# Kernel optimization log

Measured on AMD Instinct MI355X. Metric: run time of the kernel, lower is better.

Reference implementation:

```python
import jax, jax.numpy as jnp
import numpy as np

CHUNK = 32
HEADS = 4
EPS_RMS = 1e-5

def silu(x):
    return jax.nn.silu(x)

def l2norm(x, eps=1e-6):
    return x * jax.lax.rsqrt(jnp.sum(x * x, axis=-1, keepdims=True) + eps)

def short_conv(x, w):
    # x: (b, l, c); w: (c, K) depthwise causal conv, no bias
    K = w.shape[1]
    L = x.shape[1]
    xp = jnp.pad(x, ((0, 0), (K - 1, 0), (0, 0)))
    out = xp[:, 0:L, :] * w[:, 0]
    for k in range(1, K):
        out = out + xp[:, k:k + L, :] * w[:, k]
    return out

def delta_rule_chunkwise(q, k, v, beta, chunk=CHUNK):
    # q,k: (b,h,l,dk); v: (b,h,l,dv); beta: (b,h,l). l divisible by chunk.
    b, h, l, dk = q.shape
    dv = v.shape[-1]
    n = l // chunk
    q = l2norm(q)
    k = l2norm(k)
    v = v * beta[..., None]
    k_beta = k * beta[..., None]
    resh = lambda x: x.reshape(b, h, n, chunk, -1)
    q, k, v, k_beta = map(resh, (q, k, v, k_beta))
    strict_lower = jnp.tril(jnp.ones((chunk, chunk), bool), -1)
    # A = -(k_beta k^T) kept strictly lower triangular
    attn = jnp.where(strict_lower, -(k_beta @ jnp.swapaxes(k, -1, -2)), 0.0)
    # forward substitution: T = (I - A)^{-1} - I built row by row (fixed 32 rows)
    for i in range(1, chunk):
        row = attn[..., i, :]                                  # (b,h,n,c)
        new = attn[..., i, :i] + jnp.einsum('...j,...jk->...k', row, attn[..., :, :i])
        attn = attn.at[..., i, :i].set(new)
    attn = attn + jnp.eye(chunk, dtype=attn.dtype)
    u = attn @ v        # (b,h,n,c,dv)
    w = attn @ k_beta   # (b,h,n,c,dk)
    lower_incl = jnp.tril(jnp.ones((chunk, chunk), bool))
    qc, kc, uc, wc = [jnp.moveaxis(x, 2, 0) for x in (q, k, u, w)]
    S0 = jnp.zeros((b, h, dk, dv), q.dtype)
    def step(S, inp):
        q_i, k_i, u_i, w_i = inp
        attn_i = jnp.where(lower_incl, q_i @ jnp.swapaxes(k_i, -1, -2), 0.0)
        u_adj = u_i - w_i @ S
        o_i = q_i @ S + attn_i @ u_adj
        S = S + jnp.swapaxes(k_i, -1, -2) @ u_adj
        return S, o_i
    S, o = jax.lax.scan(step, S0, (qc, kc, uc, wc))
    o = jnp.moveaxis(o, 0, 2).reshape(b, h, l, dv)
    return o, S

def ema_rule(v, gamma):
    # v: (b,h,l,dv), gamma: (b,h,l); sequential EMA scan
    v_t = jnp.moveaxis(v, 2, 0)       # (l,b,h,dv)
    g_t = jnp.moveaxis(gamma, 2, 0)   # (l,b,h)
    s0 = jnp.zeros(v.shape[:2] + (v.shape[-1],), v.dtype)
    def step(s, inp):
        vt, gt = inp
        s = gt[..., None] * s + (1.0 - gt[..., None]) * vt
        return s, s
    s_fin, out = jax.lax.scan(step, s0, (v_t, g_t))
    return jnp.moveaxis(out, 0, 2), s_fin

def rms_norm(x, w, eps=EPS_RMS):
    return x * jax.lax.rsqrt(jnp.mean(x * x, axis=-1, keepdims=True) + eps) * w

def setup_inputs() -> dict:
    key = jax.random.key(0)
    ks = jax.random.split(key, 16)
    b, l, d = 4, 2048, 1024
    H, conv_K = HEADS, 4
    s = 0.02
    return {
        'hidden_states': jax.random.normal(ks[0], (b, l, d), jnp.float32),
        'Wq': jax.random.normal(ks[1], (d, d), jnp.float32) * s,
        'Wk': jax.random.normal(ks[2], (d, d), jnp.float32) * s,
        'Wv': jax.random.normal(ks[3], (d, d), jnp.float32) * s,
        'conv_q': jax.random.normal(ks[4], (d, conv_K), jnp.float32) * 0.3,
        'conv_k': jax.random.normal(ks[5], (d, conv_K), jnp.float32) * 0.3,
        'conv_v': jax.random.normal(ks[6], (d, conv_K), jnp.float32) * 0.3,
        'Wb': jax.random.normal(ks[7], (d, H), jnp.float32) * s,
        'Wdec': jax.random.normal(ks[8], (d, H), jnp.float32) * s,
        'Wmix': jax.random.normal(ks[9], (d, H), jnp.float32) * s,
        'conv_mix': jax.random.normal(ks[10], (H, conv_K), jnp.float32) * 0.3,
        'mix_bias': jnp.full((H,), -2.0, jnp.float32),
        'rms_w': jnp.ones((d // H,), jnp.float32),
        'Wo': jax.random.normal(ks[11], (d, d), jnp.float32) * s,
    }

def reference(hidden_states, Wq, Wk, Wv, conv_q, conv_k, conv_v, Wb, Wdec, Wmix, conv_mix, mix_bias, rms_w, Wo):
    b, l, d = hidden_states.shape
    H = HEADS
    dk = d // H
    dv = d // H
    # projections + causal depthwise short conv (silu activation inside conv)
    q = silu(short_conv(hidden_states @ Wq, conv_q))
    k = silu(short_conv(hidden_states @ Wk, conv_k))
    v = silu(short_conv(hidden_states @ Wv, conv_v))
    mix_inp = silu(short_conv(hidden_states @ Wmix, conv_mix))  # (b,l,H)
    # qk_activation == 'silu' applies an extra silu after conv (per source)
    q = silu(q)
    k = silu(k)
    # split heads -> (b,H,l,dh)
    to_heads = lambda x, dh: jnp.transpose(x.reshape(b, l, H, dh), (0, 2, 1, 3))
    q_d = to_heads(q, dk)
    k_d = to_heads(k, dk)
    v_d = to_heads(v, dv)
    beta = jax.nn.sigmoid(hidden_states @ Wb)           # (b,l,H)
    beta_d = jnp.transpose(beta, (0, 2, 1))             # (b,H,l)
    o_d, S = delta_rule_chunkwise(q_d, k_d, v_d, beta_d)
    o_d = jnp.transpose(o_d, (0, 2, 1, 3))              # (b,l,H,dv)
    # EMA branch
    gamma = jax.nn.sigmoid(hidden_states @ Wdec)        # (b,l,H)
    gamma_d = jnp.transpose(gamma, (0, 2, 1))
    ema_out, ema_state = ema_rule(v_d, gamma_d)
    ema_out = jnp.transpose(ema_out, (0, 2, 1, 3))      # (b,l,H,dv)
    # fine-grained head mix gate
    mix = jax.nn.sigmoid(mix_inp + mix_bias)            # (b,l,H)
    o = (1.0 - mix[..., None]) * o_d + mix[..., None] * ema_out
    # per-head RMSNorm then output projection
    o = rms_norm(o, rms_w)
    out = o.reshape(b, l, H * dv) @ Wo
    return out
```

## Files before the change

### kernel.cpp

```cpp
#include <hip/hip_runtime.h>
#include <hip/hip_bf16.h>

#define B 4
#define L 2048
#define D 1024
#define NH 4
#define DK 256
#define CHUNK 32
#define NCH 64
#define BH (B*NH)
#define ET 64
#define ENCH (L/ET)
#define TB 8

typedef __attribute__((ext_vector_type(8))) __bf16 bf16x8;
typedef __attribute__((ext_vector_type(4))) __bf16 bf16x4;
typedef __attribute__((ext_vector_type(4))) float f32x4;

__device__ inline unsigned short f2bf(float f) {
    union { float f; unsigned u; } v; v.f = f;
    unsigned r = v.u + 0x7fffu + ((v.u >> 16) & 1u);
    return (unsigned short)(r >> 16);
}
__device__ inline float bf2f(unsigned short h) {
    union { unsigned u; float f; } v; v.u = ((unsigned)h) << 16; return v.f;
}
__device__ inline float sigmoidf_(float x) { return 1.0f / (1.0f + __expf(-x)); }
__device__ inline float siluf_(float x) { return x / (1.0f + __expf(-x)); }
__device__ inline unsigned cvt_pk_bf16(float lo, float hi) {
    unsigned r;
    asm("v_cvt_pk_bf16_f32 %0, %1, %2" : "=v"(r) : "v"(lo), "v"(hi));
    return r;
}

#define MFMA16(a, b, c) __builtin_amdgcn_mfma_f32_16x16x32_bf16((a), (b), (c), 0, 0, 0)

__device__ inline void bar_lds() {
    __builtin_amdgcn_s_waitcnt(0xC07F);
    __builtin_amdgcn_s_barrier();
}

__device__ inline void load_lds16(const unsigned short* g, unsigned short* l) {
    __builtin_amdgcn_global_load_lds(
        (const __attribute__((address_space(1))) unsigned int*)g,
        (__attribute__((address_space(3))) unsigned int*)l, 16, 0, 0);
}

__global__ __launch_bounds__(256) void k_wT(const float* Wq, const float* Wk, const float* Wv,
                                            const float* Wo, unsigned short* wT)
{
    __shared__ float tile[32][33];
    int z = blockIdx.z;
    const float* W = (z == 0) ? Wq : (z == 1) ? Wk : (z == 2) ? Wv : Wo;
    unsigned short* out = wT + (size_t)z * D * D;
    int kt = blockIdx.x * 32, nt = blockIdx.y * 32;
    int tx = threadIdx.x & 31, ty = threadIdx.x >> 5;
#pragma unroll
    for (int i = 0; i < 4; i++)
        tile[ty + 8 * i][tx] = W[(size_t)(kt + ty + 8 * i) * D + nt + tx];
    __syncthreads();
#pragma unroll
    for (int i = 0; i < 4; i++)
        out[(size_t)(nt + ty + 8 * i) * D + kt + tx] = f2bf(tile[tx][ty + 8 * i]);
}

__global__ __launch_bounds__(256) void k_cvt(const float* h, unsigned short* hb, int n4)
{
    int i = blockIdx.x * blockDim.x + threadIdx.x;
    int stride = gridDim.x * blockDim.x;
    const float4* h4 = (const float4*)h;
    for (; i < n4; i += stride) {
        float4 v = h4[i];
        ushort4 o;
        o.x = f2bf(v.x); o.y = f2bf(v.y); o.z = f2bf(v.z); o.w = f2bf(v.w);
        *(ushort4*)(hb + 4 * (size_t)i) = o;
    }
}

template<int NTOT, bool OUT_F32>
__global__ __launch_bounds__(256) void k_gemm_lds(const unsigned short* __restrict__ A,
                                                  const unsigned short* __restrict__ BT,
                                                  void* __restrict__ outp)
{
    __shared__ __align__(16) unsigned short As[128 * 32];
    __shared__ __align__(16) unsigned short Bs[128 * 32];
    const int K = 1024;
    int tid = threadIdx.x;
    int w = tid >> 6, lane = tid & 63;
    int r16 = lane & 15, quad = lane >> 4;
    int wm = w & 1, wn = w >> 1;
    int bm = blockIdx.x * 128;
    int bn = blockIdx.y * 128;
    int lrow = lane >> 2;
    int lcol = (lane & 3) * 8;
    f32x4 z4 = {0.f, 0.f, 0.f, 0.f};
    f32x4 acc[4][4];
#pragma unroll
    for (int i = 0; i < 4; i++)
#pragma unroll
        for (int j = 0; j < 4; j++) acc[i][j] = z4;

    for (int kt = 0; kt < K; kt += 32) {
#pragma unroll
        for (int j = 0; j < 2; j++) {
            int r0 = (w * 2 + j) * 16;
            load_lds16(A + (size_t)(bm + r0 + lrow) * K + kt + lcol, &As[r0 * 32]);
            load_lds16(BT + (size_t)(bn + r0 + lrow) * K + kt + lcol, &Bs[r0 * 32]);
        }
        __syncthreads();
        bf16x8 af[4], bf[4];
#pragma unroll
        for (int ms = 0; ms < 4; ms++)
            af[ms] = *(const bf16x8*)&As[(wm * 64 + ms * 16 + r16) * 32 + quad * 8];
#pragma unroll
        for (int ns = 0; ns < 4; ns++)
            bf[ns] = *(const bf16x8*)&Bs[(wn * 64 + ns * 16 + r16) * 32 + quad * 8];
#pragma unroll
        for (int ms = 0; ms < 4; ms++)
#pragma unroll
            for (int ns = 0; ns < 4; ns++)
                acc[ms][ns] = MFMA16(af[ms], bf[ns], acc[ms][ns]);
        __syncthreads();
    }
#pragma unroll
    for (int ms = 0; ms < 4; ms++)
#pragma unroll
        for (int ns = 0; ns < 4; ns++)
#pragma unroll
            for (int r = 0; r < 4; r++) {
                int m = bm + wm * 64 + ms * 16 + quad * 4 + r;
                int n = bn + wn * 64 + ns * 16 + r16;
                if (OUT_F32)
                    ((float*)outp)[(size_t)m * NTOT + n] = acc[ms][ns][r];
                else
                    ((unsigned short*)outp)[(size_t)m * NTOT + n] = f2bf(acc[ms][ns][r]);
            }
}

__global__ __launch_bounds__(256) void k_smallproj(const float* hid, const float* Wb, const float* Wd,
                                                   const float* Wm, float* beta, float* gamma, float* xmix)
{
    int wave = threadIdx.x >> 6, lane = threadIdx.x & 63;
    int row = blockIdx.x * 4 + wave;
    const float* hrow = hid + (size_t)row * D;
    float acc[12];
#pragma unroll
    for (int j = 0; j < 12; j++) acc[j] = 0.f;
    for (int i = 0; i < 16; i++) {
        int k = lane + 64 * i;
        float h = hrow[k];
        float4 wb = ((const float4*)Wb)[k];
        float4 wd = ((const float4*)Wd)[k];
        float4 wm = ((const float4*)Wm)[k];
        acc[0] += h * wb.x; acc[1] += h * wb.y; acc[2] += h * wb.z; acc[3] += h * wb.w;
        acc[4] += h * wd.x; acc[5] += h * wd.y; acc[6] += h * wd.z; acc[7] += h * wd.w;
        acc[8] += h * wm.x; acc[9] += h * wm.y; acc[10] += h * wm.z; acc[11] += h * wm.w;
    }
#pragma unroll
    for (int j = 0; j < 12; j++)
        for (int off = 32; off; off >>= 1) acc[j] += __shfl_xor(acc[j], off, 64);
    if (lane < 4) {
        beta[(size_t)row * 4 + lane] = sigmoidf_(acc[lane]);
        gamma[(size_t)row * 4 + lane] = sigmoidf_(acc[4 + lane]);
        xmix[(size_t)row * 4 + lane] = acc[8 + lane];
    }
}

__global__ __launch_bounds__(256) void k_convnorm(const unsigned short* __restrict__ xqkv,
                                                  const float* __restrict__ cq,
                                                  const float* __restrict__ ck,
                                                  const float* __restrict__ cv,
                                                  unsigned short* __restrict__ qn,
                                                  unsigned short* __restrict__ kn,
                                                  unsigned short* __restrict__ vb)
{
    int blk = blockIdx.x;
    int b = blk >> 8;
    int t0 = (blk & 255) * TB;
    int tid = threadIdx.x;
    int h = tid >> 6, lane = tid & 63;
    int c = tid * 4;

    float wq[4][4], wk[4][4], wv[4][4];
#pragma unroll
    for (int j = 0; j < 4; j++) {
        float4 a = *(const float4*)(cq + (size_t)(c + j) * 4);
        wq[j][0] = a.x; wq[j][1] = a.y; wq[j][2] = a.z; wq[j][3] = a.w;
        float4 d4 = *(const float4*)(ck + (size_t)(c + j) * 4);
        wk[j][0] = d4.x; wk[j][1] = d4.y; wk[j][2] = d4.z; wk[j][3] = d4.w;
        float4 e = *(const float4*)(cv + (size_t)(c + j) * 4);
        wv[j][0] = e.x; wv[j][1] = e.y; wv[j][2] = e.z; wv[j][3] = e.w;
    }

    float aq[4][4], ak[4][4], av[4][4];
#pragma unroll
    for (int s = 0; s < 4; s++)
#pragma unroll
        for (int j = 0; j < 4; j++) { aq[s][j] = 0.f; ak[s][j] = 0.f; av[s][j] = 0.f; }

    const unsigned short* xb = xqkv + (size_t)(b * L) * (3 * D) + c;

#pragma unroll
    for (int p = 0; p < 3; p++) {
        int r = t0 - 3 + p;
        if (r >= 0) {
            const unsigned short* pp = xb + (size_t)r * (3 * D);
            ushort4 xq = *(const ushort4*)pp;
            ushort4 xk = *(const ushort4*)(pp + D);
            ushort4 xv = *(const ushort4*)(pp + 2 * D);
            float fq[4] = {bf2f(xq.x), bf2f(xq.y), bf2f(xq.z), bf2f(xq.w)};
            float fk[4] = {bf2f(xk.x), bf2f(xk.y), bf2f(xk.z), bf2f(xk.w)};
            float fv[4] = {bf2f(xv.x), bf2f(xv.y), bf2f(xv.z), bf2f(xv.w)};
#pragma unroll
            for (int d = 3 - p; d <= 3; d++) {
                int s = (p + d + 1) & 3;
                int kk = 3 - d;
#pragma unroll
                for (int j = 0; j < 4; j++) {
                    aq[s][j] += wq[j][kk] * fq[j];
                    ak[s][j] += wk[j][kk] * fk[j];
                    av[s][j] += wv[j][kk] * fv[j];
                }
            }
        }
    }

    ushort4 sq2[2], sk2[2], sv2[2];
    {
        const unsigned short* pp = xb + (size_t)t0 * (3 * D);
        sq2[0] = *(const ushort4*)pp;
        sk2[0] = *(const ushort4*)(pp + D);
        sv2[0] = *(const ushort4*)(pp + 2 * D);
    }

#pragma unroll
    for (int i = 0; i < TB; i++) {
        if (i + 1 < TB) {
            const unsigned short* pp = xb + (size_t)(t0 + i + 1) * (3 * D);
            sq2[(i + 1) & 1] = *(const ushort4*)pp;
            sk2[(i + 1) & 1] = *(const ushort4*)(pp + D);
            sv2[(i + 1) & 1] = *(const ushort4*)(pp + 2 * D);
        }
        {
            ushort4 xq = sq2[i & 1], xk = sk2[i & 1], xv = sv2[i & 1];
            float fq[4] = {bf2f(xq.x), bf2f(xq.y), bf2f(xq.z), bf2f(xq.w)};
            float fk[4] = {bf2f(xk.x), bf2f(xk.y), bf2f(xk.z), bf2f(xk.w)};
            float fv[4] = {bf2f(xv.x), bf2f(xv.y), bf2f(xv.z), bf2f(xv.w)};
#pragma unroll
            for (int d = 0; d < 4; d++) {
                if (i + d < TB) {
                    int s = (i + d) & 3;
                    int kk = 3 - d;
#pragma unroll
                    for (int j = 0; j < 4; j++) {
                        aq[s][j] += wq[j][kk] * fq[j];
                        ak[s][j] += wk[j][kk] * fk[j];
                        av[s][j] += wv[j][kk] * fv[j];
                    }
                }
            }
        }
        {
            const int s = i & 3;
            float rq[4], rk[4], rv[4];
#pragma unroll
            for (int j = 0; j < 4; j++) {
                rq[j] = siluf_(siluf_(aq[s][j]));
                rk[j] = siluf_(siluf_(ak[s][j]));
                rv[j] = siluf_(av[s][j]);
            }
            float sqs = rq[0] * rq[0] + rq[1] * rq[1] + rq[2] * rq[2] + rq[3] * rq[3];
            float sks = rk[0] * rk[0] + rk[1] * rk[1] + rk[2] * rk[2] + rk[3] * rk[3];
            for (int off = 32; off; off >>= 1) {
                sqs += __shfl_xor(sqs, off, 64);
                sks += __shfl_xor(sks, off, 64);
            }
            float qs = rsqrtf(sqs + 1e-6f), ks = rsqrtf(sks + 1e-6f);
            int t = t0 + i;
            size_t oidx = ((size_t)(b * NH + h) * L + t) * DK + lane * 4;
            ushort4 oq, ok, ov;
            oq.x = f2bf(rq[0] * qs); oq.y = f2bf(rq[1] * qs); oq.z = f2bf(rq[2] * qs); oq.w = f2bf(rq[3] * qs);
            ok.x = f2bf(rk[0] * ks); ok.y = f2bf(rk[1] * ks); ok.z = f2bf(rk[2] * ks); ok.w = f2bf(rk[3] * ks);
            ov.x = f2bf(rv[0]); ov.y = f2bf(rv[1]); ov.z = f2bf(rv[2]); ov.w = f2bf(rv[3]);
            *(ushort4*)(qn + oidx) = oq;
            *(ushort4*)(kn + oidx) = ok;
            *(ushort4*)(vb + (size_t)(b * L + t) * D + c) = ov;
            if (i + 4 < TB) {
#pragma unroll
                for (int j = 0; j < 4; j++) { aq[s][j] = 0.f; ak[s][j] = 0.f; av[s][j] = 0.f; }
            }
        }
    }
}

__global__ __launch_bounds__(256) void k_convmix(const float* xmix, const float* cmix, float* mixinp)
{
    int idx = blockIdx.x * 256 + threadIdx.x;
    int h = idx & 3;
    int t = (idx >> 2) & (L - 1);
    int b = idx >> 13;
    float acc = 0.f;
#pragma unroll
    for (int kk = 0; kk < 4; kk++) {
        int tt = t - 3 + kk;
        if (tt >= 0) acc += cmix[h * 4 + kk] * xmix[((size_t)(b * L + tt) << 2) + h];
    }
    mixinp[idx] = siluf_(acc);
}

#define KTS 40
__global__ __launch_bounds__(256) void k_delta_pre(const unsigned short* qn, const unsigned short* kn,
                                                   const unsigned short* vb, const float* beta,
                                                   unsigned short* wneg, unsigned short* knT,
                                                   unsigned short* attnb, float* u)
{
    __shared__ __align__(16) unsigned short kTl[256 * KTS];
    __shared__ __align__(16) unsigned short vTl[256 * KTS];
    __shared__ __align__(16) unsigned short T2b[32 * KTS];
    __shared__ float Gs[32 * 33];
    int bx = blockIdx.x;
    int bh = bx >> 6, ch = bx & 63;
    int b = bh >> 2, h = bh & 3;
    int t0 = ch * 32;
    int tid = threadIdx.x;
    int w = tid >> 6, lane = tid & 63;
    int r16 = lane & 15, quad = lane >> 4;
    size_t rowbase = (size_t)(bh * L + t0);
    f32x4 z4 = {0.f, 0.f, 0.f, 0.f};

    if (w < 3) {
        int mi = (w == 0) ? 0 : 1;
        int ni = (w == 2) ? 1 : 0;
        const unsigned short* krm = kn + (rowbase + mi * 16 + r16) * DK;
        const unsigned short* krn = kn + (rowbase + ni * 16 + r16) * DK;
        const unsigned short* qrm = qn + (rowbase + mi * 16 + r16) * DK;
        f32x4 g = z4, qk = z4;
#pragma unroll
        for (int kt = 0; kt < 8; kt++) {
            bf16x8 a  = *(const bf16x8*)(krm + kt * 32 + quad * 8);
            bf16x8 bb = *(const bf16x8*)(krn + kt * 32 + quad * 8);
            bf16x8 qa = *(const bf16x8*)(qrm + kt * 32 + quad * 8);
            g  = MFMA16(a, bb, g);
            qk = MFMA16(qa, bb, qk);
        }
#pragma unroll
        for (int r = 0; r < 4; r++) {
            int i = mi * 16 + quad * 4 + r, j = ni * 16 + r16;
            Gs[i * 33 + j] = g[r];
            attnb[(size_t)(bh * 64 + ch) * 1024 + i * 32 + j] =
                (j <= i) ? f2bf(qk[r]) : (unsigned short)0;
        }
    } else {
#pragma unroll
        for (int r = 0; r < 4; r++) {
            int i = quad * 4 + r, j = 16 + r16;
            attnb[(size_t)(bh * 64 + ch) * 1024 + i * 32 + j] = 0;
        }
    }
    {
        int t = tid & 31, c0 = (tid >> 5) * 32;
        const unsigned short* krow = kn + (rowbase + t) * DK + c0;
        const unsigned short* vrow = vb + ((size_t)(b * L + t0 + t)) * D + h * DK + c0;
#pragma unroll
        for (int j = 0; j < 32; j += 4) {
            ushort4 kv = *(const ushort4*)(krow + j);
            ushort4 vv = *(const ushort4*)(vrow + j);
            kTl[(c0 + j + 0) * KTS + t] = kv.x;
            kTl[(c0 + j + 1) * KTS + t] = kv.y;
            kTl[(c0 + j + 2) * KTS + t] = kv.z;
            kTl[(c0 + j + 3) * KTS + t] = kv.w;
            vTl[(c0 + j + 0) * KTS + t] = vv.x;
            vTl[(c0 + j + 1) * KTS + t] = vv.y;
            vTl[(c0 + j + 2) * KTS + t] = vv.z;
            vTl[(c0 + j + 3) * KTS + t] = vv.w;
        }
    }
    __syncthreads();

    if (w == 0) {
        int c = lane & 31;
        float rr[32];
#pragma unroll
        for (int j = 0; j < 32; j++) rr[j] = Gs[j * 33 + c];
        rr[0] = 0.f;
        float bc = beta[(size_t)(b * L + t0 + c) * NH + h];
#pragma unroll
        for (int i = 1; i < 32; i++) {
            float bi = __shfl(bc, i, 64);
            float s = -bi * rr[i];
#pragma unroll
            for (int j = 1; j < i; j++) {
                float aij = -bi * __shfl(rr[i], j, 64);
                s += aij * ((c < j) ? rr[j] : 0.f);
            }
            rr[i] = (c < i) ? s : 0.f;
        }
        if (lane < 32) {
#pragma unroll
            for (int i = 0; i < 32; i++) {
                float val = (rr[i] + ((i == c) ? 1.f : 0.f)) * bc;
                T2b[i * KTS + c] = f2bf(val);
            }
        }
    } else {
        int idx = tid - 64;
        for (int rowc = idx; rowc < 256; rowc += 192) {
            unsigned short* kT = knT + ((size_t)(bh * 64 + ch) * DK + rowc) * 32;
#pragma unroll
            for (int seg = 0; seg < 4; seg++) {
                uint4 d = *(const uint4*)&kTl[rowc * KTS + seg * 8];
                *(uint4*)(kT + seg * 8) = d;
            }
        }
    }
    __syncthreads();

#pragma unroll
    for (int mt = 0; mt < 2; mt++) {
        bf16x8 ta = *(const bf16x8*)&T2b[(mt * 16 + r16) * KTS + quad * 8];
#pragma unroll
        for (int nt2 = 0; nt2 < 4; nt2++) {
            int nt = w * 4 + nt2;
            bf16x8 vb2 = *(const bf16x8*)&vTl[(nt * 16 + r16) * KTS + quad * 8];
            bf16x8 kb = *(const bf16x8*)&kTl[(nt * 16 + r16) * KTS + quad * 8];
            f32x4 uu = MFMA16(ta, vb2, z4);
            f32x4 ww = MFMA16(ta, kb, z4);
            float* ug = u + (rowbase + mt * 16 + quad * 4) * DK + nt * 16 + r16;
            unsigned short* wg = wneg + (rowbase + mt * 16 + quad * 4) * DK + nt * 16 + r16;
#pragma unroll
            for (int r = 0; r < 4; r++) {
                ug[(size_t)r * DK] = uu[r];
                wg[(size_t)r * DK] = f2bf(-ww[r]);
            }
        }
    }
}

__global__ __launch_bounds__(256) void k_ema_local(const unsigned short* v, const float* gamma,
                                                   float* ema_local, float* Acum,
                                                   float* s_end, float* Pchunk)
{
    __shared__ float gsh[ET];
    int blk = blockIdx.x;
    int bh = blk >> 5;
    int ch = blk & (ENCH - 1);
    int b = bh >> 2, h = bh & 3;
    int c = threadIdx.x;
    int t0 = ch * ET;
    if (c < ET) gsh[c] = gamma[(size_t)(b * L + t0 + c) * NH + h];
    __syncthreads();
    const unsigned short* vg = v + (size_t)(b * L + t0) * D + h * DK + c;
    float* eg = ema_local + (size_t)(b * L + t0) * D + h * DK + c;
    float* Ag = Acum + (size_t)bh * L + t0;
    float s = 0.f;
    float A = 1.f;
#pragma unroll 8
    for (int i = 0; i < ET; i++) {
        float g = gsh[i];
        s = g * s + (1.f - g) * bf2f(vg[(size_t)i * D]);
        A *= g;
        eg[(size_t)i * D] = s;
        if (c == 0) Ag[i] = A;
    }
    s_end[((size_t)bh * ENCH + ch) * DK + c] = s;
    if (c == 0) Pchunk[(size_t)bh * ENCH + ch] = A;
}

__global__ __launch_bounds__(256) void k_ema_carry(const float* s_end, const float* Pchunk, float* S_in)
{
    int bh = blockIdx.x;
    int c = threadIdx.x;
    float S = 0.f;
    for (int ch = 0; ch < ENCH; ch++) {
        S_in[((size_t)bh * ENCH + ch) * DK + c] = S;
        float P = Pchunk[(size_t)bh * ENCH + ch];
        S = P * S + s_end[((size_t)bh * ENCH + ch) * DK + c];
    }
}

#define STS 280
#define USTR 40
__global__ __launch_bounds__(128, 1) void k_scan(const unsigned short* __restrict__ qn,
                                                 const unsigned short* __restrict__ wneg,
                                                 const unsigned short* __restrict__ knT,
                                                 const unsigned short* __restrict__ attnb,
                                                 const float* __restrict__ u, float* __restrict__ od)
{
    __shared__ __align__(16) unsigned short st[16 * STS];
    __shared__ __align__(16) unsigned short uat[16 * USTR];
    __shared__ __align__(16) unsigned short sq[2][32 * 256];
    __shared__ __align__(16) unsigned short sw[2][32 * 256];
    int bh = blockIdx.x;
    int tile = blockIdx.y;
    int b = bh >> 2, h = bh & 3;
    int mo = threadIdx.x >> 6, lane = threadIdx.x & 63;
    int n = lane & 15, q = lane >> 4;
    int cbase = tile * 16;
    f32x4 z4 = {0.f, 0.f, 0.f, 0.f};
    f32x4 sacc[8];
#pragma unroll
    for (int a = 0; a < 8; a++) sacc[a] = z4;

    const unsigned short* qb = qn + (size_t)bh * L * DK;
    const unsigned short* wb = wneg + (size_t)bh * L * DK;
    const float* ub = u + (size_t)bh * L * DK;
    const unsigned short* kTbase = knT + (size_t)bh * 64 * DK * 32;
    const unsigned short* atbase = attnb + (size_t)bh * 64 * 1024;
    int dkb = mo * 128;

    int hl = lane >> 5, cc = lane & 31;
    auto stage = [&](int ch, int p) {
        const unsigned short* src = (mo == 0) ? (qb + (size_t)ch * 32 * DK)
                                              : (wb + (size_t)ch * 32 * DK);
        unsigned short* dst = (mo == 0) ? sq[p] : sw[p];
#pragma unroll
        for (int seg = 0; seg < 16; seg++) {
            int row = seg * 2 + hl;
            int scol = cc ^ (row & 7);
            load_lds16(src + (size_t)row * DK + scol * 8, dst + seg * 512);
        }
    };

    f32x4 uB[2];
    auto loadu = [&](int ch, int p) {
        const float* up = ub + (size_t)(ch * 32 + 16 * mo + q * 4) * DK + cbase + n;
        f32x4 a; a[0] = up[0]; a[1] = up[DK]; a[2] = up[2 * DK]; a[3] = up[3 * DK];
        uB[p] = a;
    };

    bf16x8 kf2[2][8], af2[2];
    auto loadkf = [&](int ch, int p) {
        const unsigned short* kTb = kTbase + (size_t)ch * DK * 32;
#pragma unroll
        for (int a = 0; a < 8; a++)
            kf2[p][a] = *(const bf16x8*)(kTb + (size_t)(dkb + a * 16 + n) * 32 + q * 8);
        af2[p] = *(const bf16x8*)(atbase + (size_t)ch * 1024 + (16 * mo + n) * 32 + q * 8);
    };

    stage(0, 0); loadu(0, 0); loadkf(0, 0);

    auto body = [&](int ch, int par) {
        int t0 = ch * 32;
        asm volatile("s_waitcnt vmcnt(0)" ::: "memory");
        if (ch + 1 < NCH) {
            stage(ch + 1, par ^ 1);
            loadu(ch + 1, par ^ 1);
            loadkf(ch + 1, par ^ 1);
        }
#pragma unroll
        for (int a = 0; a < 8; a++) {
            uint2 pk2;
            pk2.x = cvt_pk_bf16(sacc[a][0], sacc[a][1]);
            pk2.y = cvt_pk_bf16(sacc[a][2], sacc[a][3]);
            *(uint2*)&st[n * STS + dkb + a * 16 + q * 4] = pk2;
        }
        bar_lds();

        f32x4 auE = uB[par], auO = z4, aoE = z4, aoO = z4;
        int rowoff = (16 * mo + n) * 256;
        int rsw = n & 7;
#pragma unroll
        for (int kt = 0; kt < 8; kt += 2) {
            bf16x8 s0 = *(const bf16x8*)&st[n * STS + (kt + 0) * 32 + q * 8];
            bf16x8 s1 = *(const bf16x8*)&st[n * STS + (kt + 1) * 32 + q * 8];
            bf16x8 w0 = *(const bf16x8*)&sw[par][rowoff + (((kt + 0) * 4 + q) ^ rsw) * 8];
            bf16x8 q0 = *(const bf16x8*)&sq[par][rowoff + (((kt + 0) * 4 + q) ^ rsw) * 8];
            bf16x8 w1 = *(const bf16x8*)&sw[par][rowoff + (((kt + 1) * 4 + q) ^ rsw) * 8];
            bf16x8 q1 = *(const bf16x8*)&sq[par][rowoff + (((kt + 1) * 4 + q) ^ rsw) * 8];
            auE = MFMA16(w0, s0, auE);
            aoE = MFMA16(q0, s0, aoE);
            auO = MFMA16(w1, s1, auO);
            aoO = MFMA16(q1, s1, aoO);
        }
        f32x4 au = auE + auO;

        {
            uint2 pu;
            pu.x = cvt_pk_bf16(au[0], au[1]);
            pu.y = cvt_pk_bf16(au[2], au[3]);
            *(uint2*)&uat[n * USTR + 16 * mo + q * 4] = pu;
        }
        bar_lds();

        {
            bf16x8 uf = *(const bf16x8*)&uat[n * USTR + q * 8];
            f32x4 ao = aoE + aoO;
            ao = MFMA16(af2[par], uf, ao);
            float* op = od + (size_t)(b * L + t0 + 16 * mo + q * 4) * D + h * DK + cbase + n;
            op[0] = ao[0]; op[D] = ao[1]; op[2 * D] = ao[2]; op[3 * D] = ao[3];
#pragma unroll
            for (int a = 0; a < 8; a++)
                sacc[a] = MFMA16(kf2[par][a], uf, sacc[a]);
        }
    };

    for (int ch2 = 0; ch2 < NCH; ch2 += 2) {
        body(ch2, 0);
        body(ch2 + 1, 1);
    }
}

__global__ __launch_bounds__(256) void k_mixrms(const float* od, const float* ema_local,
                                                const float* Acum, const float* S_in,
                                                const float* mixinp,
                                                const float* mix_bias, const float* rms_w,
                                                unsigned short* onorm)
{
    int row = blockIdx.x;
    int tid = threadIdx.x;
    int h = tid >> 6, lane = tid & 63;
    int b = row >> 11, t = row & (L - 1);
    int bh = b * NH + h;
    int ch = t >> 6;
    float m = sigmoidf_(mixinp[(size_t)row * NH + h] + mix_bias[h]);
    int c = tid * 4;
    float A = Acum[(size_t)bh * L + t];
    float4 sin4 = *(const float4*)(S_in + ((size_t)bh * ENCH + ch) * DK + (c & (DK - 1)));
    float4 o = *(const float4*)(od + (size_t)row * D + c);
    float4 e = *(const float4*)(ema_local + (size_t)row * D + c);
    e.x += A * sin4.x; e.y += A * sin4.y; e.z += A * sin4.z; e.w += A * sin4.w;
    float x0 = o.x + m * (e.x - o.x);
    float x1 = o.y + m * (e.y - o.y);
    float x2 = o.z + m * (e.z - o.z);
    float x3 = o.w + m * (e.w - o.w);
    float ss = x0 * x0 + x1 * x1 + x2 * x2 + x3 * x3;
    for (int off = 32; off; off >>= 1) ss += __shfl_xor(ss, off, 64);
    float scale = rsqrtf(ss * (1.0f / 256.0f) + 1e-5f);
    float4 w = *(const float4*)(rms_w + lane * 4);
    uint2 p;
    p.x = f2bf(x0 * scale * w.x) | ((unsigned)f2bf(x1 * scale * w.y) << 16);
    p.y = f2bf(x2 * scale * w.z) | ((unsigned)f2bf(x3 * scale * w.w) << 16);
    *(uint2*)(onorm + (size_t)row * D + c) = p;
}

extern "C" void kernel_launch(void* const* d_in, const int* in_sizes, int n_in,
                              void* d_out, int out_size, void* d_ws, size_t ws_size,
                              hipStream_t stream)
{
    (void)in_sizes; (void)n_in; (void)out_size; (void)ws_size;
    const float* hidden   = (const float*)d_in[0];
    const float* Wq       = (const float*)d_in[1];
    const float* Wk       = (const float*)d_in[2];
    const float* Wv       = (const float*)d_in[3];
    const float* conv_q   = (const float*)d_in[4];
    const float* conv_k   = (const float*)d_in[5];
    const float* conv_v   = (const float*)d_in[6];
    const float* Wb       = (const float*)d_in[7];
    const float* Wdec     = (const float*)d_in[8];
    const float* Wmix     = (const float*)d_in[9];
    const float* conv_mix = (const float*)d_in[10];
    const float* mix_bias = (const float*)d_in[11];
    const float* rms_w    = (const float*)d_in[12];
    const float* Wo       = (const float*)d_in[13];
    float* out = (float*)d_out;

    char* ws = (char*)d_ws;
    size_t off = 0;
    auto alloc = [&](size_t bytes) -> char* {
        char* p = ws + off;
        off += (bytes + 255) & ~(size_t)255;
        return p;
    };
    unsigned short* wT    = (unsigned short*)alloc((size_t)4 * D * D * 2);
    unsigned short* hidB  = (unsigned short*)alloc((size_t)B * L * D * 2);
    unsigned short* xqkv  = (unsigned short*)alloc((size_t)B * L * 3 * D * 2);
    float* beta   = (float*)alloc((size_t)B * L * NH * 4);
    float* gamma  = (float*)alloc((size_t)B * L * NH * 4);
    float* xmix   = (float*)alloc((size_t)B * L * NH * 4);
    float* mixinp = (float*)alloc((size_t)B * L * NH * 4);
    float* qbuf   = (float*)alloc((size_t)B * L * D * 4);
    float* kbuf   = (float*)alloc((size_t)B * L * D * 4);
    unsigned short* vb = (unsigned short*)alloc((size_t)B * L * D * 2);
    float* u      = (float*)alloc((size_t)B * L * D * 4);
    unsigned short* attnb = (unsigned short*)alloc((size_t)BH * NCH * CHUNK * CHUNK * 2);
    unsigned short* onorm = (unsigned short*)alloc((size_t)B * L * D * 2);
    unsigned short* kn    = (unsigned short*)alloc((size_t)B * L * D * 2);
    unsigned short* qn    = (unsigned short*)alloc((size_t)B * L * D * 2);
    float* Acum   = (float*)alloc((size_t)BH * L * 4);
    float* s_end  = (float*)alloc((size_t)BH * ENCH * DK * 4);
    float* Pchunk = (float*)alloc((size_t)BH * ENCH * 4);
    float* S_in   = (float*)alloc((size_t)BH * ENCH * DK * 4);

    unsigned short* wneg = xqkv + (size_t)B * L * D;
    unsigned short* knT  = xqkv + (size_t)2 * B * L * D;
    float* ema_local = qbuf;
    float* od  = kbuf;

    k_wT<<<dim3(32, 32, 4), 256, 0, stream>>>(Wq, Wk, Wv, Wo, wT);
    k_cvt<<<dim3(2048), 256, 0, stream>>>(hidden, hidB, B * L * D / 4);
    k_gemm_lds<3 * D, false><<<dim3(64, 24), 256, 0, stream>>>(hidB, wT, xqkv);
    k_smallproj<<<dim3(B * L / 4), 256, 0, stream>>>(hidden, Wb, Wdec, Wmix, beta, gamma, xmix);
    k_convnorm<<<dim3(B * L / TB), 256, 0, stream>>>(xqkv, conv_q, conv_k, conv_v, qn, kn, vb);
    k_convmix<<<dim3(B * L * NH / 256), 256, 0, stream>>>(xmix, conv_mix, mixinp);
    k_delta_pre<<<dim3(BH * NCH), 256, 0, stream>>>(qn, kn, vb, beta, wneg, knT, attnb, u);
    k_ema_local<<<dim3(BH * ENCH), 256, 0, stream>>>(vb, gamma, ema_local, Acum, s_end, Pchunk);
    k_ema_carry<<<dim3(BH), 256, 0, stream>>>(s_end, Pchunk, S_in);
    k_scan<<<dim3(16, 16), 128, 0, stream>>>(qn, wneg, knT, attnb, u, od);
    k_mixrms<<<dim3(B * L), 256, 0, stream>>>(od, ema_local, Acum, S_in, mixinp, mix_bias, rms_w, onorm);
    k_gemm_lds<D, true><<<dim3(64, 8), 256, 0, stream>>>(onorm, wT + (size_t)3 * D * D, out);
}
```

Measured before the change: 475.0 us.

## Collapse k_scan to one wavefront per block and stage kT through LDS

Rewrites the chunked delta-rule scan so a single 64-lane wavefront handles both 16-row halves of each chunk and the full 256-wide state slice. The two workgroup barriers per chunk are dropped, since all cross-lane exchange now stays inside one wave. The kT fragments are now staged into a double-buffered LDS array with async loads instead of being held in registers. The cost is that the MFMA work on the serial per-chunk path, which used to be split across two SIMDs, now runs on one. It also doubles the state accumulators per lane, adding register and LDS pressure.

Result: slower. 528.6 us (+11.3%).

```diff
diff --git a/kernel.cpp b/kernel.cpp
--- a/kernel.cpp
+++ b/kernel.cpp
@@ -480,117 +480,125 @@
 
 #define STS 280
 #define USTR 40
-__global__ __launch_bounds__(128, 1) void k_scan(const unsigned short* __restrict__ qn,
-                                                 const unsigned short* __restrict__ wneg,
-                                                 const unsigned short* __restrict__ knT,
-                                                 const unsigned short* __restrict__ attnb,
-                                                 const float* __restrict__ u, float* __restrict__ od)
-{
+__global__ __launch_bounds__(64, 1) void k_scan(const unsigned short* __restrict__ qn,
+                                                const unsigned short* __restrict__ wneg,
+                                                const unsigned short* __restrict__ knT,
+                                                const unsigned short* __restrict__ attnb,
+                                                const float* __restrict__ u, float* __restrict__ od)
+{
+    __shared__ __align__(16) unsigned short sq[2][32 * 256];
+    __shared__ __align__(16) unsigned short sw[2][32 * 256];
+    __shared__ __align__(16) unsigned short skT[2][256 * 32];
     __shared__ __align__(16) unsigned short st[16 * STS];
     __shared__ __align__(16) unsigned short uat[16 * USTR];
-    __shared__ __align__(16) unsigned short sq[2][32 * 256];
-    __shared__ __align__(16) unsigned short sw[2][32 * 256];
     int bh = blockIdx.x;
     int tile = blockIdx.y;
     int b = bh >> 2, h = bh & 3;
-    int mo = threadIdx.x >> 6, lane = threadIdx.x & 63;
+    int lane = threadIdx.x;
     int n = lane & 15, q = lane >> 4;
     int cbase = tile * 16;
     f32x4 z4 = {0.f, 0.f, 0.f, 0.f};
-    f32x4 sacc[8];
-#pragma unroll
-    for (int a = 0; a < 8; a++) sacc[a] = z4;
+    f32x4 Sacc[16];
+#pragma unroll
+    for (int i = 0; i < 16; i++) Sacc[i] = z4;
 
     const unsigned short* qb = qn + (size_t)bh * L * DK;
     const unsigned short* wb = wneg + (size_t)bh * L * DK;
     const float* ub = u + (size_t)bh * L * DK;
     const unsigned short* kTbase = knT + (size_t)bh * 64 * DK * 32;
     const unsigned short* atbase = attnb + (size_t)bh * 64 * 1024;
-    int dkb = mo * 128;
 
     int hl = lane >> 5, cc = lane & 31;
     auto stage = [&](int ch, int p) {
-        const unsigned short* src = (mo == 0) ? (qb + (size_t)ch * 32 * DK)
-                                              : (wb + (size_t)ch * 32 * DK);
-        unsigned short* dst = (mo == 0) ? sq[p] : sw[p];
+        const unsigned short* qsrc = qb + (size_t)ch * 32 * DK;
+        const unsigned short* wsrc = wb + (size_t)ch * 32 * DK;
+        const unsigned short* ksrc = kTbase + (size_t)ch * DK * 32;
 #pragma unroll
         for (int seg = 0; seg < 16; seg++) {
             int row = seg * 2 + hl;
             int scol = cc ^ (row & 7);
-            load_lds16(src + (size_t)row * DK + scol * 8, dst + seg * 512);
+            load_lds16(qsrc + (size_t)row * DK + scol * 8, sq[p] + seg * 512);
+            load_lds16(wsrc + (size_t)row * DK + scol * 8, sw[p] + seg * 512);
+            load_lds16(ksrc + (size_t)seg * 512 + lane * 8 - lane * 8 + (size_t)(seg * 16 + (lane >> 2)) * 32 + (lane & 3) * 8 - (size_t)seg * 512, skT[p] + seg * 512);
         }
     };
 
-    f32x4 uB[2];
+    f32x4 uB2[2][2];
     auto loadu = [&](int ch, int p) {
-        const float* up = ub + (size_t)(ch * 32 + 16 * mo + q * 4) * DK + cbase + n;
-        f32x4 a; a[0] = up[0]; a[1] = up[DK]; a[2] = up[2 * DK]; a[3] = up[3 * DK];
-        uB[p] = a;
+#pragma unroll
+        for (int mt = 0; mt < 2; mt++) {
+            const float* up = ub + (size_t)(ch * 32 + 16 * mt + q * 4) * DK + cbase + n;
+            f32x4 a; a[0] = up[0]; a[1] = up[DK]; a[2] = up[2 * DK]; a[3] = up[3 * DK];
+            uB2[p][mt] = a;
+        }
     };
-
-    bf16x8 kf2[2][8], af2[2];
-    auto loadkf = [&](int ch, int p) {
-        const unsigned short* kTb = kTbase + (size_t)ch * DK * 32;
-#pragma unroll
-        for (int a = 0; a < 8; a++)
-            kf2[p][a] = *(const bf16x8*)(kTb + (size_t)(dkb + a * 16 + n) * 32 + q * 8);
-        af2[p] = *(const bf16x8*)(atbase + (size_t)ch * 1024 + (16 * mo + n) * 32 + q * 8);
+    bf16x8 af2[2][2];
+    auto loadaf = [&](int ch, int p) {
+#pragma unroll
+        for (int mt = 0; mt < 2; mt++)
+            af2[p][mt] = *(const bf16x8*)(atbase + (size_t)ch * 1024 + (16 * mt + n) * 32 + q * 8);
     };
 
-    stage(0, 0); loadu(0, 0); loadkf(0, 0);
-
+    stage(0, 0); loadu(0, 0); loadaf(0, 0);
+
+    int rsw = n & 7;
     auto body = [&](int ch, int par) {
         int t0 = ch * 32;
         asm volatile("s_waitcnt vmcnt(0)" ::: "memory");
         if (ch + 1 < NCH) {
             stage(ch + 1, par ^ 1);
             loadu(ch + 1, par ^ 1);
-            loadkf(ch + 1, par ^ 1);
-        }
-#pragma unroll
-        for (int a = 0; a < 8; a++) {
+            loadaf(ch + 1, par ^ 1);
+        }
+#pragma unroll
+        for (int i = 0; i < 16; i++) {
             uint2 pk2;
-            pk2.x = cvt_pk_bf16(sacc[a][0], sacc[a][1]);
-            pk2.y = cvt_pk_bf16(sacc[a][2], sacc[a][3]);
-            *(uint2*)&st[n * STS + dkb + a * 16 + q * 4] = pk2;
-        }
-        bar_lds();
-
-        f32x4 auE = uB[par], auO = z4, aoE = z4, aoO = z4;
-        int rowoff = (16 * mo + n) * 256;
-        int rsw = n & 7;
+            pk2.x = cvt_pk_bf16(Sacc[i][0], Sacc[i][1]);
+            pk2.y = cvt_pk_bf16(Sacc[i][2], Sacc[i][3]);
+            *(uint2*)&st[n * STS + i * 16 + q * 4] = pk2;
+        }
+        f32x4 auE[2], auO[2], aoE[2], aoO[2];
+#pragma unroll
+        for (int mt = 0; mt < 2; mt++) {
+            auE[mt] = uB2[par][mt]; auO[mt] = z4; aoE[mt] = z4; aoO[mt] = z4;
+        }
 #pragma unroll
         for (int kt = 0; kt < 8; kt += 2) {
             bf16x8 s0 = *(const bf16x8*)&st[n * STS + (kt + 0) * 32 + q * 8];
             bf16x8 s1 = *(const bf16x8*)&st[n * STS + (kt + 1) * 32 + q * 8];
-            bf16x8 w0 = *(const bf16x8*)&sw[par][rowoff + (((kt + 0) * 4 + q) ^ rsw) * 8];
-            bf16x8 q0 = *(const bf16x8*)&sq[par][rowoff + (((kt + 0) * 4 + q) ^ rsw) * 8];
-            bf16x8 w1 = *(const bf16x8*)&sw[par][rowoff + (((kt + 1) * 4 + q) ^ rsw) * 8];
-            bf16x8 q1 = *(const bf16x8*)&sq[par][rowoff + (((kt + 1) * 4 + q) ^ rsw) * 8];
-            auE = MFMA16(w0, s0, auE);
-            aoE = MFMA16(q0, s0, aoE);
-            auO = MFMA16(w1, s1, auO);
-            aoO = MFMA16(q1, s1, aoO);
-        }
-        f32x4 au = auE + auO;
-
-        {
+#pragma unroll
+            for (int mt = 0; mt < 2; mt++) {
+                int rowoff = (16 * mt + n) * 256;
+                bf16x8 w0 = *(const bf16x8*)&sw[par][rowoff + (((kt + 0) * 4 + q) ^ rsw) * 8];
+                bf16x8 q0 = *(const bf16x8*)&sq[par][rowoff + (((kt + 0) * 4 + q) ^ rsw) * 8];
+                bf16x8 w1 = *(const bf16x8*)&sw[par][rowoff + (((kt + 1) * 4 + q) ^ rsw) * 8];
+                bf16x8 q1 = *(const bf16x8*)&sq[par][rowoff + (((kt + 1) * 4 + q) ^ rsw) * 8];
+                auE[mt] = MFMA16(w0, s0, auE[mt]);
+                aoE[mt] = MFMA16(q0, s0, aoE[mt]);
+                auO[mt] = MFMA16(w1, s1, auO[mt]);
+                aoO[mt] = MFMA16(q1, s1, aoO[mt]);
+            }
+        }
+#pragma unroll
+        for (int mt = 0; mt < 2; mt++) {
+            f32x4 au = auE[mt] + auO[mt];
             uint2 pu;
             pu.x = cvt_pk_bf16(au[0], au[1]);
             pu.y = cvt_pk_bf16(au[2], au[3]);
-            *(uint2*)&uat[n * USTR + 16 * mo + q * 4] = pu;
-        }
-        bar_lds();
-
-        {
-            bf16x8 uf = *(const bf16x8*)&uat[n * USTR + q * 8];
-            f32x4 ao = aoE + aoO;
-            ao = MFMA16(af2[par], uf, ao);
-            float* op = od + (size_t)(b * L + t0 + 16 * mo + q * 4) * D + h * DK + cbase + n;
+            *(uint2*)&uat[n * USTR + 16 * mt + q * 4] = pu;
+        }
+        bf16x8 uf = *(const bf16x8*)&uat[n * USTR + q * 8];
+#pragma unroll
+        for (int mt = 0; mt < 2; mt++) {
+            f32x4 ao = aoE[mt] + aoO[mt];
+            ao = MFMA16(af2[par][mt], uf, ao);
+            float* op = od + (size_t)(b * L + t0 + 16 * mt + q * 4) * D + h * DK + cbase + n;
             op[0] = ao[0]; op[D] = ao[1]; op[2 * D] = ao[2]; op[3 * D] = ao[3];
-#pragma unroll
-            for (int a = 0; a < 8; a++)
-                sacc[a] = MFMA16(kf2[par][a], uf, sacc[a]);
+        }
+#pragma unroll
+        for (int i = 0; i < 16; i++) {
+            bf16x8 kfi = *(const bf16x8*)&skT[par][(i * 16 + n) * 32 + q * 8];
+            Sacc[i] = MFMA16(kfi, uf, Sacc[i]);
         }
     };
 
@@ -695,7 +703,7 @@
     k_delta_pre<<<dim3(BH * NCH), 256, 0, stream>>>(qn, kn, vb, beta, wneg, knT, attnb, u);
     k_ema_local<<<dim3(BH * ENCH), 256, 0, stream>>>(vb, gamma, ema_local, Acum, s_end, Pchunk);
     k_ema_carry<<<dim3(BH), 256, 0, stream>>>(s_end, Pchunk, S_in);
-    k_scan<<<dim3(16, 16), 128, 0, stream>>>(qn, wneg, knT, attnb, u, od);
+    k_scan<<<dim3(16, 16), 64, 0, stream>>>(qn, wneg, knT, attnb, u, od);
     k_mixrms<<<dim3(B * L), 256, 0, stream>>>(od, ema_local, Acum, S_in, mixinp, mix_bias, rms_w, onorm);
     k_gemm_lds<D, true><<<dim3(64, 8), 256, 0, stream>>>(onorm, wT + (size_t)3 * D * D, out);
 }
```
